# Kernel tuning notes

Hardware: AMD Instinct MI355X
Metric: run time of the kernel (lower is better)

The kernel has to match this reference:

```python
import jax, jax.numpy as jnp
import numpy as np

TOK_DIM = 512
POS_DIM = 512
N_HEADS = 16
HEAD_DIM = 64
D_MODEL = 1024
INNER = N_HEADS * HEAD_DIM
B, T = 4, 2048


def setup_inputs() -> dict:
    key = jax.random.key(0)
    ks = jax.random.split(key, 5)
    s = 0.02
    return {
        "x": jax.random.normal(ks[0], (B, T, TOK_DIM + POS_DIM), dtype=jnp.float32),
        "Wq": jax.random.normal(ks[1], (POS_DIM, INNER), dtype=jnp.float32) * s,
        "Wk": jax.random.normal(ks[2], (POS_DIM, INNER), dtype=jnp.float32) * s,
        "Wv": jax.random.normal(ks[3], (TOK_DIM, INNER), dtype=jnp.float32) * s,
        "Wo": jax.random.normal(ks[4], (INNER, D_MODEL), dtype=jnp.float32) * s,
    }


def reference(x, Wq, Wk, Wv, Wo):
    b, t, _ = x.shape
    x_tok = x[:, :, :TOK_DIM]
    x_pos = x[:, :, TOK_DIM:]
    # project and split heads: [B, H, T, Dh]
    q = (x_pos @ Wq).reshape(b, t, N_HEADS, HEAD_DIM).transpose(0, 2, 1, 3)
    k = (x_pos @ Wk).reshape(b, t, N_HEADS, HEAD_DIM).transpose(0, 2, 1, 3)
    v = (x_tok @ Wv).reshape(b, t, N_HEADS, HEAD_DIM).transpose(0, 2, 1, 3)
    att = jnp.einsum("bhqd,bhkd->bhqk", q, k) / jnp.sqrt(jnp.float32(HEAD_DIM))
    causal = jnp.tril(jnp.ones((t, t), dtype=bool))
    att = jnp.where(causal, att, -jnp.inf)
    att = jax.nn.softmax(att, axis=-1)
    out = jnp.einsum("bhqk,bhkd->bhqd", att, v)
    out = out.transpose(0, 2, 1, 3).reshape(b, t, INNER)
    return out @ Wo
```

## Files before the change

kernel.cpp:

```cpp
#include <hip/hip_runtime.h>
#include <stdint.h>


typedef unsigned short u16;
typedef __bf16 bf16;
typedef bf16 bf16x8 __attribute__((ext_vector_type(8)));
typedef u16 u16x8 __attribute__((ext_vector_type(8)));
typedef u16 u16x4 __attribute__((ext_vector_type(4)));
typedef float f32x4 __attribute__((ext_vector_type(4)));
typedef uint32_t u32x4 __attribute__((ext_vector_type(4)));

__device__ __forceinline__ u16 cvt_bf16(float f) {
  uint32_t u = __builtin_bit_cast(uint32_t, f);
  u += 0x7FFFu + ((u >> 16) & 1u);
  return (u16)(u >> 16);
}

__device__ __forceinline__ uint32_t pack2_bf16(float lo, float hi) {
  uint32_t a = __builtin_bit_cast(uint32_t, lo) + 0x8000u;
  uint32_t b = __builtin_bit_cast(uint32_t, hi) + 0x8000u;
  return __builtin_amdgcn_perm(b, a, 0x07060302u);
}

__device__ __forceinline__ f32x4 mfma_bf(bf16x8 a, bf16x8 b, f32x4 c) {
  return __builtin_amdgcn_mfma_f32_16x16x32_bf16(a, b, c, 0, 0, 0);
}

typedef __attribute__((address_space(1))) const uint32_t g_u32;
typedef __attribute__((address_space(3))) uint32_t l_u32;
__device__ __forceinline__ void gload16(const u16* g, u16* l) {
  __builtin_amdgcn_global_load_lds((g_u32*)g, (l_u32*)l, 16, 0, 0);
}

__global__ __launch_bounds__(256) void prep_x(
    const float* __restrict__ x, u16* __restrict__ xtok,
    u16* __restrict__ xpos) {
  int idx = blockIdx.x * 256 + threadIdx.x;
  int row = idx >> 8;
  int c4 = (idx & 255) * 4;
  float4 v = *(const float4*)(x + (size_t)row * 1024 + c4);
  u16x4 b = {cvt_bf16(v.x), cvt_bf16(v.y), cvt_bf16(v.z), cvt_bf16(v.w)};
  u16* dst = (c4 < 512) ? (xtok + (size_t)row * 512 + c4)
                        : (xpos + (size_t)row * 512 + c4 - 512);
  *(u16x4*)dst = b;
}

__global__ __launch_bounds__(256) void prep_w(
    const float* __restrict__ Wq, const float* __restrict__ Wk,
    const float* __restrict__ Wv, const float* __restrict__ Wo,
    u16* __restrict__ Wt, u16* __restrict__ WoT) {
  const int z = blockIdx.z;
  const float* src = (z == 0) ? Wq : (z == 1) ? Wk : (z == 2) ? Wv : Wo;
  const int K = (z == 3) ? 1024 : 512;
  u16* dst = (z == 3) ? WoT : (Wt + (size_t)z * 1024 * 512);
  const int k0 = blockIdx.y * 64, n0 = blockIdx.x * 64;
  if (k0 >= K) return;
  __shared__ u16 T[64][68];
  const int tid = threadIdx.x;
  const int r = tid >> 4, c = (tid & 15) * 4;
#pragma unroll
  for (int i = 0; i < 4; i++) {
    float4 v = *(const float4*)(src + (size_t)(k0 + r + i * 16) * 1024 + n0 + c);
    u16x4 b = {cvt_bf16(v.x), cvt_bf16(v.y), cvt_bf16(v.z), cvt_bf16(v.w)};
    *(u16x4*)&T[r + i * 16][c] = b;
  }
  __syncthreads();
#pragma unroll
  for (int i = 0; i < 4; i++) {
    int n = r + i * 16;
    u16x4 v;
#pragma unroll
    for (int j = 0; j < 4; j++) v[j] = T[c + j][n];
    *(u16x4*)(dst + (size_t)(n0 + n) * K + k0 + c) = v;
  }
}


#define LDA(P, S) { const u16* bp_ = rA + (P)*16384 + (S)*8192;              \
  af[0][0] = *(const bf16x8*)(bp_ + 0*1024 + colx0);                         \
  af[0][1] = *(const bf16x8*)(bp_ + 0*1024 + colx1);                         \
  af[1][0] = *(const bf16x8*)(bp_ + 1*1024 + colx0);                         \
  af[1][1] = *(const bf16x8*)(bp_ + 1*1024 + colx1);                         \
  af[2][0] = *(const bf16x8*)(bp_ + 2*1024 + colx0);                         \
  af[2][1] = *(const bf16x8*)(bp_ + 2*1024 + colx1);                         \
  af[3][0] = *(const bf16x8*)(bp_ + 3*1024 + colx0);                         \
  af[3][1] = *(const bf16x8*)(bp_ + 3*1024 + colx1); }

#define LDB(P, S, NB) { const u16* bp_ = rB + (P)*16384 + (S)*8192;          \
  bf[(NB)+0][0] = *(const bf16x8*)(bp_ + 0*1024 + colx0);                    \
  bf[(NB)+0][1] = *(const bf16x8*)(bp_ + 0*1024 + colx1);                    \
  bf[(NB)+1][0] = *(const bf16x8*)(bp_ + 1*1024 + colx0);                    \
  bf[(NB)+1][1] = *(const bf16x8*)(bp_ + 1*1024 + colx1); }

#define MM1(M_, N_, J_) { f32x4 c_ = acc[M_][N_];                            \
  c_ = mfma_bf(af[J_][0], bf[N_][0], c_);                                    \
  c_ = mfma_bf(af[J_][1], bf[N_][1], c_);                                    \
  acc[M_][N_] = c_; }

#define MM(MB, NB) MM1((MB)+0,(NB)+0,0) MM1((MB)+0,(NB)+1,0)                 \
                   MM1((MB)+1,(NB)+0,1) MM1((MB)+1,(NB)+1,1)                 \
                   MM1((MB)+2,(NB)+0,2) MM1((MB)+2,(NB)+1,2)                 \
                   MM1((MB)+3,(NB)+0,3) MM1((MB)+3,(NB)+1,3)

#define STA(P, S, KT) { const u16* s_ = gA + (size_t)(S)*64*Kd + (KT)*64;    \
  u16* d_ = lA + (P)*16384 + (S)*8192;                                       \
  gload16(s_, d_); gload16(s_ + (size_t)128*Kd, d_ + 4096); }

#define STB(P, S, KT) { const u16* s_ = gB + (size_t)(S)*32*Kd + (KT)*64;    \
  u16* d_ = lB + (P)*16384 + (S)*8192;                                       \
  gload16(s_, d_); gload16(s_ + (size_t)128*Kd, d_ + 4096); }

#define PH_MID  asm volatile("" ::: "memory"); __builtin_amdgcn_s_barrier(); \
  asm volatile("s_waitcnt lgkmcnt(0)" ::: "memory");                         \
  __builtin_amdgcn_s_setprio(1);

#define PH_END  __builtin_amdgcn_s_setprio(0);                               \
  asm volatile("" ::: "memory"); __builtin_amdgcn_s_barrier();

#define PH_END_VM  __builtin_amdgcn_s_setprio(0);                            \
  asm volatile("s_waitcnt vmcnt(6)" ::: "memory");                           \
  asm volatile("" ::: "memory"); __builtin_amdgcn_s_barrier();

template <int Kd>
__device__ __forceinline__ void gemm256_core(
    const u16* __restrict__ Aptr, const u16* __restrict__ Bptr,
    int m0, int n0, u16* smem, f32x4 (&acc)[8][4]) {
  constexpr int NKT = Kd / 64;
  constexpr int NI = NKT / 2;
  const int tid = threadIdx.x;
  const int lane = tid & 63;
  const int mrow = lane & 15, quad = lane >> 4;
  const int w = tid >> 6, wm2 = w >> 2, wn4 = w & 3;

  u16* As = smem;
  u16* Bs = smem + 32768;

  const int lrs = tid >> 3, sp8 = tid & 7;
  const int slog = sp8 ^ (lrs & 7);
  const u16* gA = Aptr + (size_t)(m0 + (lrs & 63)) * Kd + slog * 8;
  const u16* gB =
      Bptr + (size_t)(n0 + ((lrs >> 5) << 6) + (lrs & 31)) * Kd + slog * 8;
  u16* lA = As + tid * 8;
  u16* lB = Bs + tid * 8;

  const int colx0 = (quad * 8) ^ ((mrow & 7) * 8);
  const int colx1 = (32 + quad * 8) ^ ((mrow & 7) * 8);
  const u16* rA = As + (wm2 * 64 + mrow) * 64;
  const u16* rB = Bs + (wn4 * 32 + mrow) * 64;

  bf16x8 af[4][2], bf[4][2];

  STA(0, 0, 0) STB(0, 0, 0) STB(0, 1, 0) STA(0, 1, 0)
  STA(1, 0, 1) STB(1, 0, 1) STB(1, 1, 1)
  asm volatile("s_waitcnt vmcnt(6)" ::: "memory");
  asm volatile("" ::: "memory");
  __builtin_amdgcn_s_barrier();

  for (int i = 0; i < NI; ++i) {
    const int kt1 = 2 * i + 1;
    const int kt2 = (2 * i + 2 < NKT) ? 2 * i + 2 : NKT - 1;
    const int kt3 = (2 * i + 3 < NKT) ? 2 * i + 3 : NKT - 1;
    LDA(0, 0) LDB(0, 0, 0) STA(1, 1, kt1)
    PH_MID MM(0, 0) PH_END
    LDB(0, 1, 2) STA(0, 0, kt2)
    PH_MID MM(0, 2) PH_END
    LDA(0, 1) STB(0, 0, kt2)
    PH_MID MM(4, 2) PH_END
    STB(0, 1, kt2)
    PH_MID MM(4, 0) PH_END_VM
    LDA(1, 0) LDB(1, 0, 0) STA(0, 1, kt2)
    PH_MID MM(0, 0) PH_END
    LDB(1, 1, 2) STA(1, 0, kt3)
    PH_MID MM(0, 2) PH_END
    LDA(1, 1) STB(1, 0, kt3)
    PH_MID MM(4, 2) PH_END
    STB(1, 1, kt3)
    PH_MID MM(4, 0) PH_END_VM
  }
  asm volatile("s_waitcnt vmcnt(0)" ::: "memory");
  __builtin_amdgcn_s_barrier();
}

__global__ __launch_bounds__(512, 2) void gemm_qkv256(
    const u16* __restrict__ xtok, const u16* __restrict__ xpos,
    const u16* __restrict__ Wt, u16* __restrict__ qkv,
    u16* __restrict__ vperm) {
  const int z = blockIdx.z;
  const u16* A = (z == 2) ? xtok : xpos;
  const u16* Bt = Wt + (size_t)z * 1024 * 512;
  u16* outp = qkv + (size_t)z * (64u * 2048u * 64u);
  const float osc = (z == 0) ? 0.18033688011112042f : 1.0f;
  const int m0 = blockIdx.y * 256, n0 = blockIdx.x * 256;

  __shared__ __align__(16) u16 smem[65536];
  f32x4 acc[8][4];
#pragma unroll
  for (int i = 0; i < 8; i++)
#pragma unroll
    for (int j = 0; j < 4; j++) acc[i][j] = (f32x4){0.f, 0.f, 0.f, 0.f};

  gemm256_core<512>(A, Bt, m0, n0, smem, acc);

  const int tid = threadIdx.x;
  const int lane = tid & 63;
  const int mrow = lane & 15, quad = lane >> 4;
  const int w = tid >> 6, wm2 = w >> 2, wn4 = w & 3;

  if (z != 2) {
#pragma unroll
    for (int mi = 0; mi < 8; mi++)
#pragma unroll
      for (int ni = 0; ni < 4; ni++)
#pragma unroll
        for (int r = 0; r < 4; r++) {
          int m = m0 + wm2 * 128 + mi * 16 + quad * 4 + r;
          int n = n0 + wn4 * 64 + ni * 16 + mrow;
          int bb = m >> 11, t = m & 2047;
          int h = n >> 6, d = n & 63;
          outp[(((size_t)(bb * 16 + h)) * 2048 + t) * 64 + d] =
              cvt_bf16(acc[mi][ni][r] * osc);
        }
  } else {
#pragma unroll
    for (int mi = 0; mi < 8; mi++)
#pragma unroll
      for (int ni = 0; ni < 4; ni++)
#pragma unroll
        for (int r = 0; r < 4; r++) {
          int m = m0 + wm2 * 128 + mi * 16 + quad * 4 + r;
          int n = n0 + wn4 * 64 + ni * 16 + mrow;
          int bb = m >> 11, t = m & 2047;
          int h = n >> 6, d = n & 63;
          int k6 = t & 63;
          int pos = (k6 & 32) + ((k6 >> 4) & 1) * 4 + ((k6 >> 2) & 3) * 8 +
                    (k6 & 3);
          vperm[(((size_t)(bb * 16 + h)) * 64 + d) * 2048 + (t & ~63) + pos] =
              cvt_bf16(acc[mi][ni][r]);
        }
  }
}

__global__ __launch_bounds__(512, 2) void gemm_out256(
    const u16* __restrict__ Am, const u16* __restrict__ WoT,
    float* __restrict__ out) {
  const int m0 = blockIdx.y * 256, n0 = blockIdx.x * 256;

  __shared__ __align__(16) u16 smem[65536];
  f32x4 acc[8][4];
#pragma unroll
  for (int i = 0; i < 8; i++)
#pragma unroll
    for (int j = 0; j < 4; j++) acc[i][j] = (f32x4){0.f, 0.f, 0.f, 0.f};

  gemm256_core<1024>(Am, WoT, m0, n0, smem, acc);

  const int tid = threadIdx.x;
  const int lane = tid & 63;
  const int mrow = lane & 15, quad = lane >> 4;
  const int w = tid >> 6, wm2 = w >> 2, wn4 = w & 3;

#pragma unroll
  for (int mi = 0; mi < 8; mi++)
#pragma unroll
    for (int ni = 0; ni < 4; ni++)
#pragma unroll
      for (int r = 0; r < 4; r++) {
        int m = m0 + wm2 * 128 + mi * 16 + quad * 4 + r;
        int n = n0 + wn4 * 64 + ni * 16 + mrow;
        out[(size_t)m * 1024 + n] = acc[mi][ni][r];
      }
}

__global__ __launch_bounds__(256, 4) void attn(
    const u16* __restrict__ qkv, const u16* __restrict__ vperm,
    u16* __restrict__ aout) {
  const int bh = blockIdx.x;
  const int qt = 15 - blockIdx.y;
  const int bb = bh >> 4, h = bh & 15;
  const u16* Qp = qkv + (size_t)bh * (2048 * 64);
  const u16* Kp = qkv + (size_t)(64 + bh) * (2048 * 64);
  const u16* Vp = vperm + (size_t)bh * (64 * 2048);

  __shared__ __align__(16) u16 smem[2][4][64 * 32];

  const int tid = threadIdx.x;
  const int lane = tid & 63;
  const int w = tid >> 6;
  const int mrow = lane & 15;
  const int quad = lane >> 4;
  const int srow = w * 16 + (lane >> 2);
  const int sc = (lane & 3) * 8;
  const int soff = srow * 32 + sc;

  const u16x8 onesu = {0x3F80, 0x3F80, 0x3F80, 0x3F80,
                       0x3F80, 0x3F80, 0x3F80, 0x3F80};
  const bf16x8 ones = __builtin_bit_cast(bf16x8, onesu);

  const u16* kgb = Kp + (size_t)srow * 64 + sc;
  const u16* vgb = Vp + (size_t)srow * 2048 + sc;

  const int q0 = qt * 128;
  const int nk = 2 * qt + 2;
  const int qw = q0 + w * 32;

  const u16* qbase = Qp + (size_t)(qw + mrow) * 64 + quad * 8;
  const bf16x8 qf00 = *(const bf16x8*)qbase;
  const bf16x8 qf01 = *(const bf16x8*)(qbase + 32);
  const bf16x8 qf10 = *(const bf16x8*)(qbase + 16 * 64);
  const bf16x8 qf11 = *(const bf16x8*)(qbase + 16 * 64 + 32);

  f32x4 o[2][4], ol[2];
#pragma unroll
  for (int g = 0; g < 2; ++g) {
#pragma unroll
    for (int dt = 0; dt < 4; ++dt) o[g][dt] = (f32x4){0.f, 0.f, 0.f, 0.f};
    ol[g] = (f32x4){0.f, 0.f, 0.f, 0.f};
  }

  u16x8 ka0 = *(const u16x8*)kgb;
  u16x8 ka1 = *(const u16x8*)(kgb + 32);
  u16x8 va0 = *(const u16x8*)vgb;
  u16x8 va1 = *(const u16x8*)(vgb + 32);

  for (int it = 0; it < nk; ++it) {
    u16* buf = &smem[it & 1][0][0];
    *(u16x8*)(buf + 0 * 2048 + soff) = ka0;
    *(u16x8*)(buf + 1 * 2048 + soff) = ka1;
    *(u16x8*)(buf + 2 * 2048 + soff) = va0;
    *(u16x8*)(buf + 3 * 2048 + soff) = va1;

    if (it + 1 < nk) {
      const int kn = (it + 1) * 64;
      ka0 = *(const u16x8*)(kgb + (size_t)kn * 64);
      ka1 = *(const u16x8*)(kgb + (size_t)kn * 64 + 32);
      va0 = *(const u16x8*)(vgb + kn);
      va1 = *(const u16x8*)(vgb + kn + 32);
    }

    __syncthreads();

    const int k0 = it * 64;
    if (k0 > qw + 31) continue;

    f32x4 s[2][4];
#pragma unroll
    for (int nt = 0; nt < 4; ++nt) {
      bf16x8 kf0 = *(const bf16x8*)(buf + 0 * 2048 + (nt * 16 + mrow) * 32 + quad * 8);
      bf16x8 kf1 = *(const bf16x8*)(buf + 1 * 2048 + (nt * 16 + mrow) * 32 + quad * 8);
      f32x4 z0 = (f32x4){0.f, 0.f, 0.f, 0.f};
      z0 = mfma_bf(kf0, qf00, z0);
      s[0][nt] = mfma_bf(kf1, qf01, z0);
      f32x4 z1 = (f32x4){0.f, 0.f, 0.f, 0.f};
      z1 = mfma_bf(kf0, qf10, z1);
      s[1][nt] = mfma_bf(kf1, qf11, z1);
    }

    if (k0 + 63 > qw) {
#pragma unroll
      for (int g = 0; g < 2; ++g)
#pragma unroll
        for (int nt = 0; nt < 4; ++nt)
#pragma unroll
          for (int r = 0; r < 4; ++r)
            if (k0 + nt * 16 + quad * 4 + r > qw + g * 16 + mrow)
              s[g][nt][r] = -1e30f;
    }
#pragma unroll
    for (int g = 0; g < 2; ++g)
#pragma unroll
      for (int nt = 0; nt < 4; ++nt)
#pragma unroll
        for (int r = 0; r < 4; ++r)
          s[g][nt][r] = __builtin_amdgcn_exp2f(s[g][nt][r]);

    bf16x8 pf[2][2];
#pragma unroll
    for (int g = 0; g < 2; ++g) {
      u32x4 pw0 = {pack2_bf16(s[g][0][0], s[g][0][1]),
                   pack2_bf16(s[g][0][2], s[g][0][3]),
                   pack2_bf16(s[g][1][0], s[g][1][1]),
                   pack2_bf16(s[g][1][2], s[g][1][3])};
      u32x4 pw1 = {pack2_bf16(s[g][2][0], s[g][2][1]),
                   pack2_bf16(s[g][2][2], s[g][2][3]),
                   pack2_bf16(s[g][3][0], s[g][3][1]),
                   pack2_bf16(s[g][3][2], s[g][3][3])};
      pf[g][0] = __builtin_bit_cast(bf16x8, pw0);
      pf[g][1] = __builtin_bit_cast(bf16x8, pw1);
      ol[g] = mfma_bf(ones, pf[g][0], ol[g]);
      ol[g] = mfma_bf(ones, pf[g][1], ol[g]);
    }

#pragma unroll
    for (int dt = 0; dt < 4; ++dt) {
      bf16x8 vf0 = *(const bf16x8*)(buf + 2 * 2048 + (dt * 16 + mrow) * 32 + quad * 8);
      bf16x8 vf1 = *(const bf16x8*)(buf + 3 * 2048 + (dt * 16 + mrow) * 32 + quad * 8);
      o[0][dt] = mfma_bf(vf0, pf[0][0], o[0][dt]);
      o[0][dt] = mfma_bf(vf1, pf[0][1], o[0][dt]);
      o[1][dt] = mfma_bf(vf0, pf[1][0], o[1][dt]);
      o[1][dt] = mfma_bf(vf1, pf[1][1], o[1][dt]);
    }
  }

  __syncthreads();
  u16* Osh = &smem[0][0][0];

#pragma unroll
  for (int g = 0; g < 2; ++g) {
    const float inv = 1.f / ol[g][0];
#pragma unroll
    for (int dt = 0; dt < 4; ++dt)
#pragma unroll
      for (int r = 0; r < 4; ++r)
        Osh[(w * 32 + g * 16 + mrow) * 72 + dt * 16 + quad * 4 + r] =
            cvt_bf16(o[g][dt][r] * inv);
  }
#pragma unroll
  for (int p = 0; p < 4; ++p) {
    int ql = (lane >> 3) + 8 * p;
    int ch = lane & 7;
    u16x8 v = *(const u16x8*)&Osh[(w * 32 + ql) * 72 + ch * 8];
    int t = q0 + w * 32 + ql;
    *(u16x8*)(aout + ((size_t)(bb * 2048 + t)) * 1024 + h * 64 + ch * 8) = v;
  }
}

extern "C" void kernel_launch(void* const* d_in, const int* in_sizes, int n_in,
                              void* d_out, int out_size, void* d_ws, size_t ws_size,
                              hipStream_t stream) {
  const float* x  = (const float*)d_in[0];
  const float* Wq = (const float*)d_in[1];
  const float* Wk = (const float*)d_in[2];
  const float* Wv = (const float*)d_in[3];
  const float* Wo = (const float*)d_in[4];

  u16* qkv   = (u16*)d_ws;
  u16* vperm = qkv + (size_t)3 * 64 * 2048 * 64;
  u16* aout  = vperm + (size_t)64 * 64 * 2048;
  u16* xtok  = aout + (size_t)8192 * 1024;
  u16* xpos  = xtok + (size_t)8192 * 512;
  u16* Wt    = xpos + (size_t)8192 * 512;
  u16* WoT   = Wt + (size_t)3 * 1024 * 512;
  float* out = (float*)d_out;

  prep_x<<<dim3(8192), dim3(256), 0, stream>>>(x, xtok, xpos);
  prep_w<<<dim3(16, 16, 4), dim3(256), 0, stream>>>(Wq, Wk, Wv, Wo, Wt, WoT);
  gemm_qkv256<<<dim3(4, 32, 3), dim3(512), 0, stream>>>(xtok, xpos, Wt, qkv, vperm);
  attn<<<dim3(64, 16), dim3(256), 0, stream>>>(qkv, vperm, aout);
  gemm_out256<<<dim3(4, 32), dim3(512), 0, stream>>>(aout, WoT, out);
}
```

Measured before the change: 208.2 us.

## Double attention query tile per block to 256 rows for more K/V reuse

Each attention block now handles 256 query rows, with each wave doing 64 rows instead of 32, so every K/V tile staged in shared memory feeds twice as many MFMAs. The grid shrinks from 1024 to 512 blocks and launch bounds drop to 2 blocks per SM to leave room for the larger accumulator set. The epilogue is rewritten as two passes through a per-wave shared-memory staging area with vectorized writes. The trade-offs are higher register pressure, lower occupancy and worse causal load balance across fewer, larger blocks.

```diff
diff --git a/kernel.cpp b/kernel.cpp
--- a/kernel.cpp
+++ b/kernel.cpp
@@ -271,11 +271,11 @@
       }
 }
 
-__global__ __launch_bounds__(256, 4) void attn(
+__global__ __launch_bounds__(256, 2) void attn(
     const u16* __restrict__ qkv, const u16* __restrict__ vperm,
     u16* __restrict__ aout) {
   const int bh = blockIdx.x;
-  const int qt = 15 - blockIdx.y;
+  const int qt = 7 - blockIdx.y;
   const int bb = bh >> 4, h = bh & 15;
   const u16* Qp = qkv + (size_t)bh * (2048 * 64);
   const u16* Kp = qkv + (size_t)(64 + bh) * (2048 * 64);
@@ -299,19 +299,21 @@
   const u16* kgb = Kp + (size_t)srow * 64 + sc;
   const u16* vgb = Vp + (size_t)srow * 2048 + sc;
 
-  const int q0 = qt * 128;
-  const int nk = 2 * qt + 2;
-  const int qw = q0 + w * 32;
+  const int q0 = qt * 256;
+  const int nk = 4 * qt + 4;
+  const int qw = q0 + w * 64;
 
   const u16* qbase = Qp + (size_t)(qw + mrow) * 64 + quad * 8;
-  const bf16x8 qf00 = *(const bf16x8*)qbase;
-  const bf16x8 qf01 = *(const bf16x8*)(qbase + 32);
-  const bf16x8 qf10 = *(const bf16x8*)(qbase + 16 * 64);
-  const bf16x8 qf11 = *(const bf16x8*)(qbase + 16 * 64 + 32);
-
-  f32x4 o[2][4], ol[2];
-#pragma unroll
-  for (int g = 0; g < 2; ++g) {
+  bf16x8 qf[4][2];
+#pragma unroll
+  for (int g = 0; g < 4; ++g) {
+    qf[g][0] = *(const bf16x8*)(qbase + g * 16 * 64);
+    qf[g][1] = *(const bf16x8*)(qbase + g * 16 * 64 + 32);
+  }
+
+  f32x4 o[4][4], ol[4];
+#pragma unroll
+  for (int g = 0; g < 4; ++g) {
 #pragma unroll
     for (int dt = 0; dt < 4; ++dt) o[g][dt] = (f32x4){0.f, 0.f, 0.f, 0.f};
     ol[g] = (f32x4){0.f, 0.f, 0.f, 0.f};
@@ -340,24 +342,24 @@
     __syncthreads();
 
     const int k0 = it * 64;
-    if (k0 > qw + 31) continue;
-
-    f32x4 s[2][4];
+    if (k0 > qw + 63) continue;
+
+    f32x4 s[4][4];
 #pragma unroll
     for (int nt = 0; nt < 4; ++nt) {
       bf16x8 kf0 = *(const bf16x8*)(buf + 0 * 2048 + (nt * 16 + mrow) * 32 + quad * 8);
       bf16x8 kf1 = *(const bf16x8*)(buf + 1 * 2048 + (nt * 16 + mrow) * 32 + quad * 8);
-      f32x4 z0 = (f32x4){0.f, 0.f, 0.f, 0.f};
-      z0 = mfma_bf(kf0, qf00, z0);
-      s[0][nt] = mfma_bf(kf1, qf01, z0);
-      f32x4 z1 = (f32x4){0.f, 0.f, 0.f, 0.f};
-      z1 = mfma_bf(kf0, qf10, z1);
-      s[1][nt] = mfma_bf(kf1, qf11, z1);
+#pragma unroll
+      for (int g = 0; g < 4; ++g) {
+        f32x4 z = (f32x4){0.f, 0.f, 0.f, 0.f};
+        z = mfma_bf(kf0, qf[g][0], z);
+        s[g][nt] = mfma_bf(kf1, qf[g][1], z);
+      }
     }
 
     if (k0 + 63 > qw) {
 #pragma unroll
-      for (int g = 0; g < 2; ++g)
+      for (int g = 0; g < 4; ++g)
 #pragma unroll
         for (int nt = 0; nt < 4; ++nt)
 #pragma unroll
@@ -366,16 +368,16 @@
               s[g][nt][r] = -1e30f;
     }
 #pragma unroll
-    for (int g = 0; g < 2; ++g)
+    for (int g = 0; g < 4; ++g)
 #pragma unroll
       for (int nt = 0; nt < 4; ++nt)
 #pragma unroll
         for (int r = 0; r < 4; ++r)
           s[g][nt][r] = __builtin_amdgcn_exp2f(s[g][nt][r]);
 
-    bf16x8 pf[2][2];
-#pragma unroll
-    for (int g = 0; g < 2; ++g) {
+    bf16x8 pf[4][2];
+#pragma unroll
+    for (int g = 0; g < 4; ++g) {
       u32x4 pw0 = {pack2_bf16(s[g][0][0], s[g][0][1]),
                    pack2_bf16(s[g][0][2], s[g][0][3]),
                    pack2_bf16(s[g][1][0], s[g][1][1]),
@@ -394,33 +396,38 @@
     for (int dt = 0; dt < 4; ++dt) {
       bf16x8 vf0 = *(const bf16x8*)(buf + 2 * 2048 + (dt * 16 + mrow) * 32 + quad * 8);
       bf16x8 vf1 = *(const bf16x8*)(buf + 3 * 2048 + (dt * 16 + mrow) * 32 + quad * 8);
-      o[0][dt] = mfma_bf(vf0, pf[0][0], o[0][dt]);
-      o[0][dt] = mfma_bf(vf1, pf[0][1], o[0][dt]);
-      o[1][dt] = mfma_bf(vf0, pf[1][0], o[1][dt]);
-      o[1][dt] = mfma_bf(vf1, pf[1][1], o[1][dt]);
+#pragma unroll
+      for (int g = 0; g < 4; ++g) {
+        o[g][dt] = mfma_bf(vf0, pf[g][0], o[g][dt]);
+        o[g][dt] = mfma_bf(vf1, pf[g][1], o[g][dt]);
+      }
     }
   }
 
   __syncthreads();
-  u16* Osh = &smem[0][0][0];
-
-#pragma unroll
-  for (int g = 0; g < 2; ++g) {
-    const float inv = 1.f / ol[g][0];
-#pragma unroll
-    for (int dt = 0; dt < 4; ++dt)
-#pragma unroll
-      for (int r = 0; r < 4; ++r)
-        Osh[(w * 32 + g * 16 + mrow) * 72 + dt * 16 + quad * 4 + r] =
-            cvt_bf16(o[g][dt][r] * inv);
-  }
-#pragma unroll
-  for (int p = 0; p < 4; ++p) {
-    int ql = (lane >> 3) + 8 * p;
-    int ch = lane & 7;
-    u16x8 v = *(const u16x8*)&Osh[(w * 32 + ql) * 72 + ch * 8];
-    int t = q0 + w * 32 + ql;
-    *(u16x8*)(aout + ((size_t)(bb * 2048 + t)) * 1024 + h * 64 + ch * 8) = v;
+  u16* Osh = &smem[0][0][0] + w * 4096;
+
+#pragma unroll
+  for (int pass = 0; pass < 2; ++pass) {
+#pragma unroll
+    for (int gl = 0; gl < 2; ++gl) {
+      const int g = pass * 2 + gl;
+      const float inv = 1.f / ol[g][0];
+#pragma unroll
+      for (int dt = 0; dt < 4; ++dt) {
+        u16x4 b = {cvt_bf16(o[g][dt][0] * inv), cvt_bf16(o[g][dt][1] * inv),
+                   cvt_bf16(o[g][dt][2] * inv), cvt_bf16(o[g][dt][3] * inv)};
+        *(u16x4*)&Osh[(gl * 16 + mrow) * 72 + dt * 16 + quad * 4] = b;
+      }
+    }
+#pragma unroll
+    for (int p = 0; p < 4; ++p) {
+      int ql = (lane >> 3) + 8 * p;
+      int ch = lane & 7;
+      u16x8 v = *(const u16x8*)&Osh[ql * 72 + ch * 8];
+      int t = q0 + w * 64 + pass * 32 + ql;
+      *(u16x8*)(aout + ((size_t)(bb * 2048 + t)) * 1024 + h * 64 + ch * 8) = v;
+    }
   }
 }
 
@@ -445,6 +452,6 @@
   prep_x<<<dim3(8192), dim3(256), 0, stream>>>(x, xtok, xpos);
   prep_w<<<dim3(16, 16, 4), dim3(256), 0, stream>>>(Wq, Wk, Wv, Wo, Wt, WoT);
   gemm_qkv256<<<dim3(4, 32, 3), dim3(512), 0, stream>>>(xtok, xpos, Wt, qkv, vperm);
-  attn<<<dim3(64, 16), dim3(256), 0, stream>>>(qkv, vperm, aout);
+  attn<<<dim3(64, 8), dim3(256), 0, stream>>>(qkv, vperm, aout);
   gemm_out256<<<dim3(4, 32), dim3(512), 0, stream>>>(aout, WoT, out);
 }
```

Measured after the change: 208.4 us. Within noise of the previous version (+0.1%).

## Shrink GEMM tiles to 128x256 with new pipeline and XCD-aware block remap

Applied to the files above, without the earlier changes.

Replaces the 256x256 GEMM core used by the QKV and output projections with a 128x256 tile that has a reworked LDS staging and prefetch schedule, using fewer accumulators and less shared memory. The block grid doubles and block indices are remapped so neighbouring tiles land on the same XCD for L2 reuse. The goal is more blocks for better CU fill and tail balance on 256 CUs, at the cost of lower arithmetic intensity per tile. Launch bounds drop to one block per CU for the GEMMs and to 3 for attention.

```diff
diff --git a/kernel.cpp b/kernel.cpp
--- a/kernel.cpp
+++ b/kernel.cpp
@@ -76,7 +76,16 @@
 }
 
 
-#define LDA(P, S) { const u16* bp_ = rA + (P)*16384 + (S)*8192;              \
+#define MM1(M_, N_, J_) { f32x4 c_ = acc[M_][N_];                            \
+  c_ = mfma_bf(af[J_][0], bf[N_][0], c_);                                    \
+  c_ = mfma_bf(af[J_][1], bf[N_][1], c_);                                    \
+  acc[M_][N_] = c_; }
+
+#define XMM(NB) MM1(0,(NB)+0,0) MM1(0,(NB)+1,0) MM1(1,(NB)+0,1)              \
+                MM1(1,(NB)+1,1) MM1(2,(NB)+0,2) MM1(2,(NB)+1,2)              \
+                MM1(3,(NB)+0,3) MM1(3,(NB)+1,3)
+
+#define XLDA(P) { const u16* bp_ = rA + (P)*8192;                            \
   af[0][0] = *(const bf16x8*)(bp_ + 0*1024 + colx0);                         \
   af[0][1] = *(const bf16x8*)(bp_ + 0*1024 + colx1);                         \
   af[1][0] = *(const bf16x8*)(bp_ + 1*1024 + colx0);                         \
@@ -86,29 +95,23 @@
   af[3][0] = *(const bf16x8*)(bp_ + 3*1024 + colx0);                         \
   af[3][1] = *(const bf16x8*)(bp_ + 3*1024 + colx1); }
 
-#define LDB(P, S, NB) { const u16* bp_ = rB + (P)*16384 + (S)*8192;          \
-  bf[(NB)+0][0] = *(const bf16x8*)(bp_ + 0*1024 + colx0);                    \
-  bf[(NB)+0][1] = *(const bf16x8*)(bp_ + 0*1024 + colx1);                    \
-  bf[(NB)+1][0] = *(const bf16x8*)(bp_ + 1*1024 + colx0);                    \
-  bf[(NB)+1][1] = *(const bf16x8*)(bp_ + 1*1024 + colx1); }
-
-#define MM1(M_, N_, J_) { f32x4 c_ = acc[M_][N_];                            \
-  c_ = mfma_bf(af[J_][0], bf[N_][0], c_);                                    \
-  c_ = mfma_bf(af[J_][1], bf[N_][1], c_);                                    \
-  acc[M_][N_] = c_; }
-
-#define MM(MB, NB) MM1((MB)+0,(NB)+0,0) MM1((MB)+0,(NB)+1,0)                 \
-                   MM1((MB)+1,(NB)+0,1) MM1((MB)+1,(NB)+1,1)                 \
-                   MM1((MB)+2,(NB)+0,2) MM1((MB)+2,(NB)+1,2)                 \
-                   MM1((MB)+3,(NB)+0,3) MM1((MB)+3,(NB)+1,3)
-
-#define STA(P, S, KT) { const u16* s_ = gA + (size_t)(S)*64*Kd + (KT)*64;    \
-  u16* d_ = lA + (P)*16384 + (S)*8192;                                       \
-  gload16(s_, d_); gload16(s_ + (size_t)128*Kd, d_ + 4096); }
-
-#define STB(P, S, KT) { const u16* s_ = gB + (size_t)(S)*32*Kd + (KT)*64;    \
-  u16* d_ = lB + (P)*16384 + (S)*8192;                                       \
-  gload16(s_, d_); gload16(s_ + (size_t)128*Kd, d_ + 4096); }
+#define XLDB(P, NB) { const u16* bp_ = rB + (P)*16384;                       \
+  bf[(NB)+0][0] = *(const bf16x8*)(bp_ + ((NB)+0)*1024 + colx0);             \
+  bf[(NB)+0][1] = *(const bf16x8*)(bp_ + ((NB)+0)*1024 + colx1);             \
+  bf[(NB)+1][0] = *(const bf16x8*)(bp_ + ((NB)+1)*1024 + colx0);             \
+  bf[(NB)+1][1] = *(const bf16x8*)(bp_ + ((NB)+1)*1024 + colx1); }
+
+#define XSTA(P, KT) { const u16* s_ = gA + (KT)*64;                          \
+  u16* d_ = lA + (P)*8192;                                                   \
+  gload16(s_, d_); gload16(s_ + (size_t)64*Kd, d_ + 4096); }
+
+#define XSTB0(P, KT) { const u16* s_ = gB + (KT)*64;                         \
+  u16* d_ = lB + (P)*16384;                                                  \
+  gload16(s_, d_); gload16(s_ + (size_t)64*Kd, d_ + 4096); }
+
+#define XSTB1(P, KT) { const u16* s_ = gB + (size_t)128*Kd + (KT)*64;        \
+  u16* d_ = lB + (P)*16384 + 8192;                                           \
+  gload16(s_, d_); gload16(s_ + (size_t)64*Kd, d_ + 4096); }
 
 #define PH_MID  asm volatile("" ::: "memory"); __builtin_amdgcn_s_barrier(); \
   asm volatile("s_waitcnt lgkmcnt(0)" ::: "memory");                         \
@@ -117,14 +120,18 @@
 #define PH_END  __builtin_amdgcn_s_setprio(0);                               \
   asm volatile("" ::: "memory"); __builtin_amdgcn_s_barrier();
 
-#define PH_END_VM  __builtin_amdgcn_s_setprio(0);                            \
-  asm volatile("s_waitcnt vmcnt(6)" ::: "memory");                           \
+#define PH_END_VM2  __builtin_amdgcn_s_setprio(0);                           \
+  asm volatile("s_waitcnt vmcnt(2)" ::: "memory");                           \
   asm volatile("" ::: "memory"); __builtin_amdgcn_s_barrier();
 
+#define PH_END_VM4  __builtin_amdgcn_s_setprio(0);                           \
+  asm volatile("s_waitcnt vmcnt(4)" ::: "memory");                           \
+  asm volatile("" ::: "memory"); __builtin_amdgcn_s_barrier();
+
 template <int Kd>
-__device__ __forceinline__ void gemm256_core(
+__device__ __forceinline__ void gemm128_core(
     const u16* __restrict__ Aptr, const u16* __restrict__ Bptr,
-    int m0, int n0, u16* smem, f32x4 (&acc)[8][4]) {
+    int m0, int n0, u16* smem, f32x4 (&acc)[4][4]) {
   constexpr int NKT = Kd / 64;
   constexpr int NI = NKT / 2;
   const int tid = threadIdx.x;
@@ -132,27 +139,23 @@
   const int mrow = lane & 15, quad = lane >> 4;
   const int w = tid >> 6, wm2 = w >> 2, wn4 = w & 3;
 
-  u16* As = smem;
-  u16* Bs = smem + 32768;
-
   const int lrs = tid >> 3, sp8 = tid & 7;
   const int slog = sp8 ^ (lrs & 7);
-  const u16* gA = Aptr + (size_t)(m0 + (lrs & 63)) * Kd + slog * 8;
-  const u16* gB =
-      Bptr + (size_t)(n0 + ((lrs >> 5) << 6) + (lrs & 31)) * Kd + slog * 8;
-  u16* lA = As + tid * 8;
-  u16* lB = Bs + tid * 8;
+  const u16* gA = Aptr + (size_t)(m0 + lrs) * Kd + slog * 8;
+  const u16* gB = Bptr + (size_t)(n0 + lrs) * Kd + slog * 8;
+  u16* lA = smem + tid * 8;
+  u16* lB = smem + 16384 + tid * 8;
 
   const int colx0 = (quad * 8) ^ ((mrow & 7) * 8);
   const int colx1 = (32 + quad * 8) ^ ((mrow & 7) * 8);
-  const u16* rA = As + (wm2 * 64 + mrow) * 64;
-  const u16* rB = Bs + (wn4 * 32 + mrow) * 64;
+  const u16* rA = smem + (wm2 * 64 + mrow) * 64;
+  const u16* rB = smem + 16384 + (wn4 >> 1) * 8192 + ((wn4 & 1) * 64 + mrow) * 64;
 
   bf16x8 af[4][2], bf[4][2];
 
-  STA(0, 0, 0) STB(0, 0, 0) STB(0, 1, 0) STA(0, 1, 0)
-  STA(1, 0, 1) STB(1, 0, 1) STB(1, 1, 1)
-  asm volatile("s_waitcnt vmcnt(6)" ::: "memory");
+  XSTA(0, 0) XSTB0(0, 0) XSTB1(0, 0)
+  XSTA(1, 1) XSTB0(1, 1)
+  asm volatile("s_waitcnt vmcnt(4)" ::: "memory");
   asm volatile("" ::: "memory");
   __builtin_amdgcn_s_barrier();
 
@@ -160,28 +163,27 @@
     const int kt1 = 2 * i + 1;
     const int kt2 = (2 * i + 2 < NKT) ? 2 * i + 2 : NKT - 1;
     const int kt3 = (2 * i + 3 < NKT) ? 2 * i + 3 : NKT - 1;
-    LDA(0, 0) LDB(0, 0, 0) STA(1, 1, kt1)
-    PH_MID MM(0, 0) PH_END
-    LDB(0, 1, 2) STA(0, 0, kt2)
-    PH_MID MM(0, 2) PH_END
-    LDA(0, 1) STB(0, 0, kt2)
-    PH_MID MM(4, 2) PH_END
-    STB(0, 1, kt2)
-    PH_MID MM(4, 0) PH_END_VM
-    LDA(1, 0) LDB(1, 0, 0) STA(0, 1, kt2)
-    PH_MID MM(0, 0) PH_END
-    LDB(1, 1, 2) STA(1, 0, kt3)
-    PH_MID MM(0, 2) PH_END
-    LDA(1, 1) STB(1, 0, kt3)
-    PH_MID MM(4, 2) PH_END
-    STB(1, 1, kt3)
-    PH_MID MM(4, 0) PH_END_VM
+    XLDA(0) XLDB(0, 0) XSTB1(1, kt1)
+    PH_MID XMM(0) PH_END
+    XLDB(0, 2) XSTA(0, kt2)
+    PH_MID XMM(2) PH_END_VM2
+    XLDA(1) XLDB(1, 0) XSTB0(0, kt2)
+    PH_MID XMM(0) PH_END
+    XLDB(1, 2) XSTB1(0, kt2) XSTA(1, kt3) XSTB0(1, kt3)
+    PH_MID XMM(2) PH_END_VM4
   }
   asm volatile("s_waitcnt vmcnt(0)" ::: "memory");
   __builtin_amdgcn_s_barrier();
 }
 
-__global__ __launch_bounds__(512, 2) void gemm_qkv256(
+__device__ __forceinline__ void xcd_remap(int& bx, int& by) {
+  int flat = blockIdx.x + 4 * blockIdx.y;
+  int wg = (flat & 7) * 32 + (flat >> 3);
+  bx = wg & 3;
+  by = wg >> 2;
+}
+
+__global__ __launch_bounds__(512, 1) void gemm_qkv128(
     const u16* __restrict__ xtok, const u16* __restrict__ xpos,
     const u16* __restrict__ Wt, u16* __restrict__ qkv,
     u16* __restrict__ vperm) {
@@ -190,16 +192,18 @@
   const u16* Bt = Wt + (size_t)z * 1024 * 512;
   u16* outp = qkv + (size_t)z * (64u * 2048u * 64u);
   const float osc = (z == 0) ? 0.18033688011112042f : 1.0f;
-  const int m0 = blockIdx.y * 256, n0 = blockIdx.x * 256;
-
-  __shared__ __align__(16) u16 smem[65536];
-  f32x4 acc[8][4];
-#pragma unroll
-  for (int i = 0; i < 8; i++)
+  int bx, by;
+  xcd_remap(bx, by);
+  const int m0 = by * 128, n0 = bx * 256;
+
+  __shared__ __align__(16) u16 smem[49152];
+  f32x4 acc[4][4];
+#pragma unroll
+  for (int i = 0; i < 4; i++)
 #pragma unroll
     for (int j = 0; j < 4; j++) acc[i][j] = (f32x4){0.f, 0.f, 0.f, 0.f};
 
-  gemm256_core<512>(A, Bt, m0, n0, smem, acc);
+  gemm128_core<512>(A, Bt, m0, n0, smem, acc);
 
   const int tid = threadIdx.x;
   const int lane = tid & 63;
@@ -208,12 +212,12 @@
 
   if (z != 2) {
 #pragma unroll
-    for (int mi = 0; mi < 8; mi++)
+    for (int mi = 0; mi < 4; mi++)
 #pragma unroll
       for (int ni = 0; ni < 4; ni++)
 #pragma unroll
         for (int r = 0; r < 4; r++) {
-          int m = m0 + wm2 * 128 + mi * 16 + quad * 4 + r;
+          int m = m0 + wm2 * 64 + mi * 16 + quad * 4 + r;
           int n = n0 + wn4 * 64 + ni * 16 + mrow;
           int bb = m >> 11, t = m & 2047;
           int h = n >> 6, d = n & 63;
@@ -222,12 +226,12 @@
         }
   } else {
 #pragma unroll
-    for (int mi = 0; mi < 8; mi++)
+    for (int mi = 0; mi < 4; mi++)
 #pragma unroll
       for (int ni = 0; ni < 4; ni++)
 #pragma unroll
         for (int r = 0; r < 4; r++) {
-          int m = m0 + wm2 * 128 + mi * 16 + quad * 4 + r;
+          int m = m0 + wm2 * 64 + mi * 16 + quad * 4 + r;
           int n = n0 + wn4 * 64 + ni * 16 + mrow;
           int bb = m >> 11, t = m & 2047;
           int h = n >> 6, d = n & 63;
@@ -240,19 +244,21 @@
   }
 }
 
-__global__ __launch_bounds__(512, 2) void gemm_out256(
+__global__ __launch_bounds__(512, 1) void gemm_out128(
     const u16* __restrict__ Am, const u16* __restrict__ WoT,
     float* __restrict__ out) {
-  const int m0 = blockIdx.y * 256, n0 = blockIdx.x * 256;
-
-  __shared__ __align__(16) u16 smem[65536];
-  f32x4 acc[8][4];
-#pragma unroll
-  for (int i = 0; i < 8; i++)
+  int bx, by;
+  xcd_remap(bx, by);
+  const int m0 = by * 128, n0 = bx * 256;
+
+  __shared__ __align__(16) u16 smem[49152];
+  f32x4 acc[4][4];
+#pragma unroll
+  for (int i = 0; i < 4; i++)
 #pragma unroll
     for (int j = 0; j < 4; j++) acc[i][j] = (f32x4){0.f, 0.f, 0.f, 0.f};
 
-  gemm256_core<1024>(Am, WoT, m0, n0, smem, acc);
+  gemm128_core<1024>(Am, WoT, m0, n0, smem, acc);
 
   const int tid = threadIdx.x;
   const int lane = tid & 63;
@@ -260,18 +266,18 @@
   const int w = tid >> 6, wm2 = w >> 2, wn4 = w & 3;
 
 #pragma unroll
-  for (int mi = 0; mi < 8; mi++)
+  for (int mi = 0; mi < 4; mi++)
 #pragma unroll
     for (int ni = 0; ni < 4; ni++)
 #pragma unroll
       for (int r = 0; r < 4; r++) {
-        int m = m0 + wm2 * 128 + mi * 16 + quad * 4 + r;
+        int m = m0 + wm2 * 64 + mi * 16 + quad * 4 + r;
         int n = n0 + wn4 * 64 + ni * 16 + mrow;
         out[(size_t)m * 1024 + n] = acc[mi][ni][r];
       }
 }
 
-__global__ __launch_bounds__(256, 4) void attn(
+__global__ __launch_bounds__(256, 3) void attn(
     const u16* __restrict__ qkv, const u16* __restrict__ vperm,
     u16* __restrict__ aout) {
   const int bh = blockIdx.x;
@@ -444,7 +450,7 @@
 
   prep_x<<<dim3(8192), dim3(256), 0, stream>>>(x, xtok, xpos);
   prep_w<<<dim3(16, 16, 4), dim3(256), 0, stream>>>(Wq, Wk, Wv, Wo, Wt, WoT);
-  gemm_qkv256<<<dim3(4, 32, 3), dim3(512), 0, stream>>>(xtok, xpos, Wt, qkv, vperm);
+  gemm_qkv128<<<dim3(4, 64, 3), dim3(512), 0, stream>>>(xtok, xpos, Wt, qkv, vperm);
   attn<<<dim3(64, 16), dim3(256), 0, stream>>>(qkv, vperm, aout);
-  gemm_out256<<<dim3(4, 32), dim3(512), 0, stream>>>(aout, WoT, out);
-}
+  gemm_out128<<<dim3(4, 64), dim3(512), 0, stream>>>(aout, WoT, out);
+}
```

Result: faster. 193.3 us (-7.2%).
